# Optimization experiments

Hardware: AMD Instinct MI355X
Metric: run time of the kernel (lower is better)

## Reference

```python
import jax, jax.numpy as jnp
import numpy as np

B, C, F = 8, 2048, 128


def setup_inputs() -> dict:
    key = jax.random.key(0)
    ks = jax.random.split(key, 13)
    features = jax.random.normal(ks[0], (B, C, F), dtype=jnp.float32)
    # sparse-ish boolean adjacency masks over operations
    pred_mask = jax.random.uniform(ks[1], (B, C, C)) < 0.05
    succ_mask = jax.random.uniform(ks[2], (B, C, C)) < 0.05
    same_type_mask = jax.random.uniform(ks[3], (B, C, C)) < 0.10

    def linear(k, fan_in, fan_out):
        kw, kb = jax.random.split(k)
        bound = 1.0 / np.sqrt(fan_in)
        W = jax.random.uniform(kw, (fan_in, fan_out), minval=-bound, maxval=bound, dtype=jnp.float32)
        b = jax.random.uniform(kb, (fan_out,), minval=-bound, maxval=bound, dtype=jnp.float32)
        return W, b

    W_enc, b_enc = linear(ks[4], F, 4 * F)
    W_space, b_space = linear(ks[5], 3 * F, F)
    W_same, b_same = linear(ks[6], 2 * F, F)
    W_mix, b_mix = linear(ks[7], 2 * F, F)
    return {
        "features": features,
        "pred_mask": pred_mask,
        "succ_mask": succ_mask,
        "same_type_mask": same_type_mask,
        "W_enc": W_enc, "b_enc": b_enc,
        "W_space": W_space, "b_space": b_space,
        "W_same": W_same, "b_same": b_same,
        "W_mix": W_mix, "b_mix": b_mix,
    }


def reference(features, pred_mask, succ_mask, same_type_mask,
              W_enc, b_enc, W_space, b_space, W_same, b_same, W_mix, b_mix):
    # encoder: [B,C,F] -> [B,C,4F], split into origin + 3 message features
    enc = features @ W_enc + b_enc
    origin, e_pred, e_succ, e_same = jnp.split(enc, 4, axis=-1)

    def masked_mean(mask, e):
        # original builds (B,C,C,F) broadcast product then sums over 'other';
        # mathematically this is mask @ e with a clamped-degree divisor.
        m = mask.astype(e.dtype)                         # [B,C,C]
        deg = jnp.maximum(m.sum(-1, keepdims=True), 1.0)  # [B,C,1]
        return jnp.einsum('bij,bjf->bif', m, e) / deg

    pred_f = masked_mean(pred_mask, e_pred)
    succ_f = masked_mean(succ_mask, e_succ)
    same_f = masked_mean(same_type_mask, e_same)

    space_mixed = jnp.concatenate([pred_f, origin, succ_f], axis=-1) @ W_space + b_space
    same_mixed = jnp.concatenate([origin, same_f], axis=-1) @ W_same + b_same
    return jnp.concatenate([space_mixed, same_mixed], axis=-1) @ W_mix + b_mix
```

## Files before the change

### kernel.cpp

```cpp
#include <hip/hip_runtime.h>
#include <stdint.h>

typedef unsigned int uint;
typedef unsigned short ushort;
typedef unsigned char uchar;
typedef __attribute__((ext_vector_type(8))) short bf16x8;
typedef __attribute__((ext_vector_type(4))) float f32x4;

__device__ __forceinline__ ushort f2bf(float f) {
  uint u = __builtin_bit_cast(uint, f);
  return (ushort)((u + 0x7FFFu + ((u >> 16) & 1u)) >> 16);
}

__global__ __launch_bounds__(256) void k_detect(
    const uint* __restrict__ m, int* __restrict__ esz_out) {
  __shared__ int s_ok;
  if (threadIdx.x == 0) s_ok = 1;
  __syncthreads();
  int ok = 1;
  for (int i = 0; i < 64; ++i) {
    uint v = m[(size_t)threadIdx.x * 64 + i];
    if (!(v == 0u || v == 1u || v == 0x3F800000u)) ok = 0;
  }
  if (!ok) atomicAnd(&s_ok, 0);
  __syncthreads();
  if (threadIdx.x == 0) *esz_out = s_ok ? 4 : 1;
}

__global__ __launch_bounds__(256) void k_cvt_feat(
    const float4* __restrict__ in, ushort* __restrict__ out) {
  for (int i = blockIdx.x * 256 + threadIdx.x; i < 524288; i += 65536) {
    float4 v = in[i];
    ushort4 o;
    o.x = f2bf(v.x); o.y = f2bf(v.y); o.z = f2bf(v.z); o.w = f2bf(v.w);
    *(ushort4*)&out[(size_t)i * 4] = o;
  }
}

__global__ __launch_bounds__(256) void k_twt(
    const float* __restrict__ We, const float* __restrict__ Ws,
    const float* __restrict__ Wm, const float* __restrict__ Wx,
    ushort* __restrict__ Te, ushort* __restrict__ Ts,
    ushort* __restrict__ Tm, ushort* __restrict__ Tx) {
  int i = blockIdx.x * 256 + threadIdx.x;
  if (i < 65536) { int n = i >> 7, k = i & 127; Te[i] = f2bf(We[k * 512 + n]); return; }
  i -= 65536;
  if (i < 49152) { int n = i / 384, k = i - n * 384; Ts[i] = f2bf(Ws[k * 128 + n]); return; }
  i -= 49152;
  if (i < 32768) { int n = i >> 8, k = i & 255; Tm[i] = f2bf(Wm[k * 128 + n]); return; }
  i -= 32768;
  if (i < 32768) { int n = i >> 8, k = i & 255; Tx[i] = f2bf(Wx[k * 128 + n]); return; }
}

__device__ __forceinline__ void mfma_tiles(const ushort* As, const ushort* Bs,
                                           int m0w, int n0w, int lr, int quad,
                                           f32x4 acc[2][4]) {
#pragma unroll
  for (int kc = 0; kc < 2; ++kc) {
    bf16x8 a[2], b[4];
#pragma unroll
    for (int i = 0; i < 2; ++i)
      a[i] = *(const bf16x8*)&As[(m0w + i * 16 + lr) * 72 + kc * 32 + quad * 8];
#pragma unroll
    for (int j = 0; j < 4; ++j)
      b[j] = *(const bf16x8*)&Bs[(n0w + j * 16 + lr) * 72 + kc * 32 + quad * 8];
#pragma unroll
    for (int i = 0; i < 2; ++i)
#pragma unroll
      for (int j = 0; j < 4; ++j)
        acc[i][j] = __builtin_amdgcn_mfma_f32_16x16x32_bf16(a[i], b[j], acc[i][j], 0, 0, 0);
  }
}

__global__ __launch_bounds__(256) void k_enc(
    const ushort* __restrict__ featbf, const ushort* __restrict__ WTe,
    const float* __restrict__ bias, ushort* __restrict__ origin,
    ushort* __restrict__ eT0, ushort* __restrict__ eT1, ushort* __restrict__ eT2) {
  __shared__ ushort As[64 * 72];
  __shared__ ushort Bs[128 * 72];
  const int t = threadIdx.x;
  const int gm0 = blockIdx.x * 64;
  const int y = blockIdx.y;
  const ushort* Bsrc = WTe + (size_t)y * 128 * 128;
  const int lane = t & 63, wave = t >> 6;
  const int m0w = (wave >> 1) * 32, n0w = (wave & 1) * 64;
  const int quad = lane >> 4, lr = lane & 15;
  const int am = t >> 2, aq = t & 3;
  const int bn = t >> 1, bh = t & 1;
  f32x4 acc[2][4] = {};
  for (int k0 = 0; k0 < 128; k0 += 64) {
    const ushort* asrc = featbf + (size_t)(gm0 + am) * 128 + k0 + aq * 16;
    bf16x8 av0 = *(const bf16x8*)asrc;
    bf16x8 av1 = *(const bf16x8*)(asrc + 8);
    const ushort* bsrc = Bsrc + (size_t)bn * 128 + k0 + bh * 32;
    bf16x8 bv0 = *(const bf16x8*)bsrc;
    bf16x8 bv1 = *(const bf16x8*)(bsrc + 8);
    bf16x8 bv2 = *(const bf16x8*)(bsrc + 16);
    bf16x8 bv3 = *(const bf16x8*)(bsrc + 24);
    *(bf16x8*)&As[am * 72 + aq * 16] = av0;
    *(bf16x8*)&As[am * 72 + aq * 16 + 8] = av1;
    *(bf16x8*)&Bs[bn * 72 + bh * 32] = bv0;
    *(bf16x8*)&Bs[bn * 72 + bh * 32 + 8] = bv1;
    *(bf16x8*)&Bs[bn * 72 + bh * 32 + 16] = bv2;
    *(bf16x8*)&Bs[bn * 72 + bh * 32 + 24] = bv3;
    __syncthreads();
    mfma_tiles(As, Bs, m0w, n0w, lr, quad, acc);
    __syncthreads();
  }
  ushort* eT = (y == 1) ? eT0 : (y == 2) ? eT1 : eT2;
#pragma unroll
  for (int i = 0; i < 2; ++i)
#pragma unroll
    for (int j = 0; j < 4; ++j)
#pragma unroll
      for (int r = 0; r < 4; ++r) {
        int m = gm0 + m0w + i * 16 + quad * 4 + r;
        int n = n0w + j * 16 + lr;
        ushort h = f2bf(acc[i][j][r] + bias[y * 128 + n]);
        if (y == 0) origin[(size_t)m * 128 + n] = h;
        else eT[(size_t)n * 16384 + m] = h;
      }
}

__global__ __launch_bounds__(256) void k_mm(
    const void* __restrict__ mp, const void* __restrict__ ms, const void* __restrict__ mt,
    const ushort* __restrict__ eT0, const ushort* __restrict__ eT1, const ushort* __restrict__ eT2,
    ushort* __restrict__ P, ushort* __restrict__ S, ushort* __restrict__ T,
    const int* __restrict__ esz_p) {
  __shared__ ushort As[64 * 72];
  __shared__ ushort Bs[128 * 72];
  __shared__ uint degs[64];
  const int t = threadIdx.x;
  const int mtile = blockIdx.x, b = blockIdx.y, mid = blockIdx.z;
  const void* mask = (mid == 0) ? mp : (mid == 1) ? ms : mt;
  const ushort* eT = (mid == 0) ? eT0 : (mid == 1) ? eT1 : eT2;
  ushort* outp = (mid == 0) ? P : (mid == 1) ? S : T;
  const int esz = *esz_p;
  if (t < 64) degs[t] = 0;
  const size_t rowbase = (size_t)b * 2048 + mtile * 64;
  const int lane = t & 63, wave = t >> 6;
  const int m0w = (wave >> 1) * 32, n0w = (wave & 1) * 64;
  const int quad = lane >> 4, lr = lane & 15;
  const int am = t >> 2, aq = t & 3;
  const int bn = t >> 1, bh = t & 1;
  const ushort* bsrc_base = eT + (size_t)bn * 16384 + (size_t)b * 2048 + bh * 32;
  f32x4 acc[2][4] = {};
  int cnt = 0;
  for (int k0 = 0; k0 < 2048; k0 += 64) {
    bf16x8 o0, o1;
    if (esz == 4) {
      const uint* p = (const uint*)mask + (rowbase + am) * 2048 + k0 + aq * 16;
      uint w[16];
      *(uint4*)&w[0] = *(const uint4*)p;
      *(uint4*)&w[4] = *(const uint4*)(p + 4);
      *(uint4*)&w[8] = *(const uint4*)(p + 8);
      *(uint4*)&w[12] = *(const uint4*)(p + 12);
#pragma unroll
      for (int e = 0; e < 8; ++e) { int nz = (w[e] != 0u); o0[e] = nz ? (short)0x3F80 : (short)0; cnt += nz; }
#pragma unroll
      for (int e = 0; e < 8; ++e) { int nz = (w[e + 8] != 0u); o1[e] = nz ? (short)0x3F80 : (short)0; cnt += nz; }
    } else {
      const uchar* p = (const uchar*)mask + (rowbase + am) * 2048 + k0 + aq * 16;
      uint4 wb = *(const uint4*)p;
      uint arr[4] = {wb.x, wb.y, wb.z, wb.w};
#pragma unroll
      for (int e = 0; e < 8; ++e) { int nz = (((arr[e >> 2] >> ((e & 3) * 8)) & 0xFFu) != 0u); o0[e] = nz ? (short)0x3F80 : (short)0; cnt += nz; }
#pragma unroll
      for (int e = 0; e < 8; ++e) { int ee = e + 8; int nz = (((arr[ee >> 2] >> ((ee & 3) * 8)) & 0xFFu) != 0u); o1[e] = nz ? (short)0x3F80 : (short)0; cnt += nz; }
    }
    const ushort* bsrc = bsrc_base + k0;
    bf16x8 bv0 = *(const bf16x8*)bsrc;
    bf16x8 bv1 = *(const bf16x8*)(bsrc + 8);
    bf16x8 bv2 = *(const bf16x8*)(bsrc + 16);
    bf16x8 bv3 = *(const bf16x8*)(bsrc + 24);
    *(bf16x8*)&As[am * 72 + aq * 16] = o0;
    *(bf16x8*)&As[am * 72 + aq * 16 + 8] = o1;
    *(bf16x8*)&Bs[bn * 72 + bh * 32] = bv0;
    *(bf16x8*)&Bs[bn * 72 + bh * 32 + 8] = bv1;
    *(bf16x8*)&Bs[bn * 72 + bh * 32 + 16] = bv2;
    *(bf16x8*)&Bs[bn * 72 + bh * 32 + 24] = bv3;
    __syncthreads();
    mfma_tiles(As, Bs, m0w, n0w, lr, quad, acc);
    __syncthreads();
  }
  atomicAdd(&degs[am], (uint)cnt);
  __syncthreads();
#pragma unroll
  for (int i = 0; i < 2; ++i)
#pragma unroll
    for (int r = 0; r < 4; ++r) {
      int ml = m0w + i * 16 + quad * 4 + r;
      uint d = degs[ml];
      float inv = 1.0f / (float)(d > 0u ? d : 1u);
#pragma unroll
      for (int j = 0; j < 4; ++j) {
        int n = n0w + j * 16 + lr;
        outp[(rowbase + ml) * 128 + n] = f2bf(acc[i][j][r] * inv);
      }
    }
}

__global__ __launch_bounds__(256) void k_gemm(
    const ushort* __restrict__ A0, const ushort* __restrict__ A1,
    const ushort* __restrict__ A2, const ushort* __restrict__ Bsrc,
    int bstride, int K, const float* __restrict__ bias,
    void* __restrict__ out, int out_f32) {
  __shared__ ushort As[64 * 72];
  __shared__ ushort Bs[128 * 72];
  const int t = threadIdx.x;
  const int gm0 = blockIdx.x * 64;
  const int lane = t & 63, wave = t >> 6;
  const int m0w = (wave >> 1) * 32, n0w = (wave & 1) * 64;
  const int quad = lane >> 4, lr = lane & 15;
  const int am = t >> 2, aq = t & 3;
  const int bn = t >> 1, bh = t & 1;
  f32x4 acc[2][4] = {};
  for (int k0 = 0; k0 < K; k0 += 64) {
    const int seg = k0 >> 7;
    const ushort* Ap = (seg == 0) ? A0 : (seg == 1) ? A1 : A2;
    const ushort* asrc = Ap + (size_t)(gm0 + am) * 128 + (k0 & 127) + aq * 16;
    bf16x8 av0 = *(const bf16x8*)asrc;
    bf16x8 av1 = *(const bf16x8*)(asrc + 8);
    const ushort* bsrc = Bsrc + (size_t)bn * bstride + k0 + bh * 32;
    bf16x8 bv0 = *(const bf16x8*)bsrc;
    bf16x8 bv1 = *(const bf16x8*)(bsrc + 8);
    bf16x8 bv2 = *(const bf16x8*)(bsrc + 16);
    bf16x8 bv3 = *(const bf16x8*)(bsrc + 24);
    *(bf16x8*)&As[am * 72 + aq * 16] = av0;
    *(bf16x8*)&As[am * 72 + aq * 16 + 8] = av1;
    *(bf16x8*)&Bs[bn * 72 + bh * 32] = bv0;
    *(bf16x8*)&Bs[bn * 72 + bh * 32 + 8] = bv1;
    *(bf16x8*)&Bs[bn * 72 + bh * 32 + 16] = bv2;
    *(bf16x8*)&Bs[bn * 72 + bh * 32 + 24] = bv3;
    __syncthreads();
    mfma_tiles(As, Bs, m0w, n0w, lr, quad, acc);
    __syncthreads();
  }
#pragma unroll
  for (int i = 0; i < 2; ++i)
#pragma unroll
    for (int j = 0; j < 4; ++j)
#pragma unroll
      for (int r = 0; r < 4; ++r) {
        int m = gm0 + m0w + i * 16 + quad * 4 + r;
        int n = n0w + j * 16 + lr;
        float v = acc[i][j][r] + bias[n];
        if (out_f32) ((float*)out)[(size_t)m * 128 + n] = v;
        else ((ushort*)out)[(size_t)m * 128 + n] = f2bf(v);
      }
}

extern "C" void kernel_launch(void* const* d_in, const int* in_sizes, int n_in,
                              void* d_out, int out_size, void* d_ws,
                              size_t ws_size, hipStream_t stream) {
  const float* features = (const float*)d_in[0];
  const void* pred = d_in[1];
  const void* succ = d_in[2];
  const void* same = d_in[3];
  const float* W_enc = (const float*)d_in[4];
  const float* b_enc = (const float*)d_in[5];
  const float* W_space = (const float*)d_in[6];
  const float* b_space = (const float*)d_in[7];
  const float* W_same = (const float*)d_in[8];
  const float* b_same = (const float*)d_in[9];
  const float* W_mix = (const float*)d_in[10];
  const float* b_mix = (const float*)d_in[11];

  const size_t M = 16384;
  ushort* w = (ushort*)d_ws;
  ushort* feat_bf = w;  w += M * 128;
  ushort* WT_enc = w;   w += 512 * 128;
  ushort* WT_space = w; w += 128 * 384;
  ushort* WT_same = w;  w += 128 * 256;
  ushort* WT_mix = w;   w += 128 * 256;
  ushort* origin = w;   w += M * 128;
  ushort* eT0 = w;      w += M * 128;
  ushort* eT1 = w;      w += M * 128;
  ushort* eT2 = w;      w += M * 128;
  ushort* P = w;        w += M * 128;
  ushort* S = w;        w += M * 128;
  ushort* T = w;        w += M * 128;
  ushort* X = w;        w += M * 128;
  ushort* Y = w;        w += M * 128;
  int* esz = (int*)w;

  k_detect<<<1, 256, 0, stream>>>((const uint*)pred, esz);
  k_cvt_feat<<<256, 256, 0, stream>>>((const float4*)features, feat_bf);
  k_twt<<<704, 256, 0, stream>>>(W_enc, W_space, W_same, W_mix,
                                 WT_enc, WT_space, WT_same, WT_mix);
  k_enc<<<dim3(256, 4), 256, 0, stream>>>(feat_bf, WT_enc, b_enc,
                                          origin, eT0, eT1, eT2);
  k_mm<<<dim3(32, 8, 3), 256, 0, stream>>>(pred, succ, same, eT0, eT1, eT2,
                                           P, S, T, esz);
  k_gemm<<<256, 256, 0, stream>>>(P, origin, S, WT_space, 384, 384,
                                  b_space, X, 0);
  k_gemm<<<256, 256, 0, stream>>>(origin, T, nullptr, WT_same, 256, 256,
                                  b_same, Y, 0);
  k_gemm<<<256, 256, 0, stream>>>(X, Y, nullptr, WT_mix, 256, 256,
                                  b_mix, d_out, 1);
}
```

Measured before the change: 475.4 us.

## Drop LDS staging, load MFMA fragments directly from global, merge small kernels

Every GEMM kernel (encoder, masked aggregation, output projections) now loads bf16 fragments straight from global memory into registers instead of staging tiles through shared memory, which removes the __syncthreads barriers. The mask matmul converts byte masks to bf16 with byte-permute arithmetic, prefetches the next mask chunk, and computes degrees with wave shuffles instead of shared-memory atomics. Feature conversion and weight transposition merge into one prep kernel, and the space and same GEMMs merge into one launch. The trade-off is that operands are no longer shared between waves, so redundant global loads rely on cache hits.

```diff
diff --git a/kernel.cpp b/kernel.cpp
--- a/kernel.cpp
+++ b/kernel.cpp
@@ -12,37 +12,68 @@
   return (ushort)((u + 0x7FFFu + ((u >> 16) & 1u)) >> 16);
 }
 
+__device__ __forceinline__ bf16x8 cvt8(uint lo, uint hi, uint& cacc) {
+  uint x0 = __builtin_amdgcn_perm(0u, lo, 0x04010400u);
+  uint x1 = __builtin_amdgcn_perm(0u, lo, 0x04030402u);
+  uint x2 = __builtin_amdgcn_perm(0u, hi, 0x04010400u);
+  uint x3 = __builtin_amdgcn_perm(0u, hi, 0x04030402u);
+  uint n0 = ((x0 + 0x00FF00FFu) >> 8) & 0x00010001u;
+  uint n1 = ((x1 + 0x00FF00FFu) >> 8) & 0x00010001u;
+  uint n2 = ((x2 + 0x00FF00FFu) >> 8) & 0x00010001u;
+  uint n3 = ((x3 + 0x00FF00FFu) >> 8) & 0x00010001u;
+  cacc += n0 + n1 + n2 + n3;
+  uint4 o;
+  o.x = n0 * 0x3F80u; o.y = n1 * 0x3F80u;
+  o.z = n2 * 0x3F80u; o.w = n3 * 0x3F80u;
+  return __builtin_bit_cast(bf16x8, o);
+}
+
+__device__ __forceinline__ bf16x8 cvt8w(uint4 a, uint4 b, uint& cnt) {
+  bf16x8 r;
+  r[0] = a.x ? (short)0x3F80 : (short)0; cnt += (a.x != 0u);
+  r[1] = a.y ? (short)0x3F80 : (short)0; cnt += (a.y != 0u);
+  r[2] = a.z ? (short)0x3F80 : (short)0; cnt += (a.z != 0u);
+  r[3] = a.w ? (short)0x3F80 : (short)0; cnt += (a.w != 0u);
+  r[4] = b.x ? (short)0x3F80 : (short)0; cnt += (b.x != 0u);
+  r[5] = b.y ? (short)0x3F80 : (short)0; cnt += (b.y != 0u);
+  r[6] = b.z ? (short)0x3F80 : (short)0; cnt += (b.z != 0u);
+  r[7] = b.w ? (short)0x3F80 : (short)0; cnt += (b.w != 0u);
+  return r;
+}
+
 __global__ __launch_bounds__(256) void k_detect(
-    const uint* __restrict__ m, int* __restrict__ esz_out) {
+    const uint4* __restrict__ m, int* __restrict__ esz_out) {
   __shared__ int s_ok;
   if (threadIdx.x == 0) s_ok = 1;
   __syncthreads();
   int ok = 1;
-  for (int i = 0; i < 64; ++i) {
-    uint v = m[(size_t)threadIdx.x * 64 + i];
-    if (!(v == 0u || v == 1u || v == 0x3F800000u)) ok = 0;
+#pragma unroll
+  for (int i = 0; i < 16; ++i) {
+    uint4 v = m[i * 256 + threadIdx.x];
+    if (!(v.x <= 1u || v.x == 0x3F800000u)) ok = 0;
+    if (!(v.y <= 1u || v.y == 0x3F800000u)) ok = 0;
+    if (!(v.z <= 1u || v.z == 0x3F800000u)) ok = 0;
+    if (!(v.w <= 1u || v.w == 0x3F800000u)) ok = 0;
   }
   if (!ok) atomicAnd(&s_ok, 0);
   __syncthreads();
   if (threadIdx.x == 0) *esz_out = s_ok ? 4 : 1;
 }
 
-__global__ __launch_bounds__(256) void k_cvt_feat(
-    const float4* __restrict__ in, ushort* __restrict__ out) {
-  for (int i = blockIdx.x * 256 + threadIdx.x; i < 524288; i += 65536) {
-    float4 v = in[i];
-    ushort4 o;
-    o.x = f2bf(v.x); o.y = f2bf(v.y); o.z = f2bf(v.z); o.w = f2bf(v.w);
-    *(ushort4*)&out[(size_t)i * 4] = o;
-  }
-}
-
-__global__ __launch_bounds__(256) void k_twt(
+__global__ __launch_bounds__(256) void k_prep(
+    const float4* __restrict__ fin, ushort* __restrict__ fout,
     const float* __restrict__ We, const float* __restrict__ Ws,
     const float* __restrict__ Wm, const float* __restrict__ Wx,
     ushort* __restrict__ Te, ushort* __restrict__ Ts,
     ushort* __restrict__ Tm, ushort* __restrict__ Tx) {
-  int i = blockIdx.x * 256 + threadIdx.x;
+  const int tid = blockIdx.x * 256 + threadIdx.x;
+  for (int i = tid; i < 524288; i += 180224) {
+    float4 v = fin[i];
+    ushort4 o;
+    o.x = f2bf(v.x); o.y = f2bf(v.y); o.z = f2bf(v.z); o.w = f2bf(v.w);
+    *(ushort4*)&fout[(size_t)i * 4] = o;
+  }
+  int i = tid;
   if (i < 65536) { int n = i >> 7, k = i & 127; Te[i] = f2bf(We[k * 512 + n]); return; }
   i -= 65536;
   if (i < 49152) { int n = i / 384, k = i - n * 384; Ts[i] = f2bf(Ws[k * 128 + n]); return; }
@@ -52,83 +83,73 @@
   if (i < 32768) { int n = i >> 8, k = i & 255; Tx[i] = f2bf(Wx[k * 128 + n]); return; }
 }
 
-__device__ __forceinline__ void mfma_tiles(const ushort* As, const ushort* Bs,
-                                           int m0w, int n0w, int lr, int quad,
-                                           f32x4 acc[2][4]) {
-#pragma unroll
-  for (int kc = 0; kc < 2; ++kc) {
-    bf16x8 a[2], b[4];
-#pragma unroll
-    for (int i = 0; i < 2; ++i)
-      a[i] = *(const bf16x8*)&As[(m0w + i * 16 + lr) * 72 + kc * 32 + quad * 8];
-#pragma unroll
-    for (int j = 0; j < 4; ++j)
-      b[j] = *(const bf16x8*)&Bs[(n0w + j * 16 + lr) * 72 + kc * 32 + quad * 8];
-#pragma unroll
-    for (int i = 0; i < 2; ++i)
-#pragma unroll
-      for (int j = 0; j < 4; ++j)
-        acc[i][j] = __builtin_amdgcn_mfma_f32_16x16x32_bf16(a[i], b[j], acc[i][j], 0, 0, 0);
-  }
-}
-
 __global__ __launch_bounds__(256) void k_enc(
     const ushort* __restrict__ featbf, const ushort* __restrict__ WTe,
     const float* __restrict__ bias, ushort* __restrict__ origin,
     ushort* __restrict__ eT0, ushort* __restrict__ eT1, ushort* __restrict__ eT2) {
-  __shared__ ushort As[64 * 72];
-  __shared__ ushort Bs[128 * 72];
   const int t = threadIdx.x;
   const int gm0 = blockIdx.x * 64;
   const int y = blockIdx.y;
-  const ushort* Bsrc = WTe + (size_t)y * 128 * 128;
   const int lane = t & 63, wave = t >> 6;
   const int m0w = (wave >> 1) * 32, n0w = (wave & 1) * 64;
   const int quad = lane >> 4, lr = lane & 15;
-  const int am = t >> 2, aq = t & 3;
-  const int bn = t >> 1, bh = t & 1;
+  const ushort* a0p = featbf + (size_t)(gm0 + m0w + lr) * 128 + quad * 8;
+  const ushort* a1p = a0p + 16 * 128;
+  bf16x8 af0[4], af1[4];
+#pragma unroll
+  for (int kc = 0; kc < 4; ++kc) {
+    af0[kc] = *(const bf16x8*)(a0p + kc * 32);
+    af1[kc] = *(const bf16x8*)(a1p + kc * 32);
+  }
   f32x4 acc[2][4] = {};
-  for (int k0 = 0; k0 < 128; k0 += 64) {
-    const ushort* asrc = featbf + (size_t)(gm0 + am) * 128 + k0 + aq * 16;
-    bf16x8 av0 = *(const bf16x8*)asrc;
-    bf16x8 av1 = *(const bf16x8*)(asrc + 8);
-    const ushort* bsrc = Bsrc + (size_t)bn * 128 + k0 + bh * 32;
-    bf16x8 bv0 = *(const bf16x8*)bsrc;
-    bf16x8 bv1 = *(const bf16x8*)(bsrc + 8);
-    bf16x8 bv2 = *(const bf16x8*)(bsrc + 16);
-    bf16x8 bv3 = *(const bf16x8*)(bsrc + 24);
-    *(bf16x8*)&As[am * 72 + aq * 16] = av0;
-    *(bf16x8*)&As[am * 72 + aq * 16 + 8] = av1;
-    *(bf16x8*)&Bs[bn * 72 + bh * 32] = bv0;
-    *(bf16x8*)&Bs[bn * 72 + bh * 32 + 8] = bv1;
-    *(bf16x8*)&Bs[bn * 72 + bh * 32 + 16] = bv2;
-    *(bf16x8*)&Bs[bn * 72 + bh * 32 + 24] = bv3;
-    __syncthreads();
-    mfma_tiles(As, Bs, m0w, n0w, lr, quad, acc);
-    __syncthreads();
-  }
-  ushort* eT = (y == 1) ? eT0 : (y == 2) ? eT1 : eT2;
-#pragma unroll
-  for (int i = 0; i < 2; ++i)
-#pragma unroll
-    for (int j = 0; j < 4; ++j)
-#pragma unroll
-      for (int r = 0; r < 4; ++r) {
-        int m = gm0 + m0w + i * 16 + quad * 4 + r;
+#pragma unroll
+  for (int j = 0; j < 4; ++j) {
+    const ushort* bp = WTe + (size_t)(y * 128 + n0w + j * 16 + lr) * 128 + quad * 8;
+#pragma unroll
+    for (int kc = 0; kc < 4; ++kc) {
+      bf16x8 bv = *(const bf16x8*)(bp + kc * 32);
+      acc[0][j] = __builtin_amdgcn_mfma_f32_16x16x32_bf16(af0[kc], bv, acc[0][j], 0, 0, 0);
+      acc[1][j] = __builtin_amdgcn_mfma_f32_16x16x32_bf16(af1[kc], bv, acc[1][j], 0, 0, 0);
+    }
+  }
+  if (y == 0) {
+#pragma unroll
+    for (int i = 0; i < 2; ++i)
+#pragma unroll
+      for (int j = 0; j < 4; ++j) {
         int n = n0w + j * 16 + lr;
-        ushort h = f2bf(acc[i][j][r] + bias[y * 128 + n]);
-        if (y == 0) origin[(size_t)m * 128 + n] = h;
-        else eT[(size_t)n * 16384 + m] = h;
-      }
-}
-
-__global__ __launch_bounds__(256) void k_mm(
-    const void* __restrict__ mp, const void* __restrict__ ms, const void* __restrict__ mt,
-    const ushort* __restrict__ eT0, const ushort* __restrict__ eT1, const ushort* __restrict__ eT2,
+        float bb = bias[n];
+        int mb = gm0 + m0w + i * 16 + quad * 4;
+#pragma unroll
+        for (int r = 0; r < 4; ++r)
+          origin[(size_t)(mb + r) * 128 + n] = f2bf(acc[i][j][r] + bb);
+      }
+  } else {
+    ushort* eT = (y == 1) ? eT0 : (y == 2) ? eT1 : eT2;
+#pragma unroll
+    for (int i = 0; i < 2; ++i)
+#pragma unroll
+      for (int j = 0; j < 4; ++j) {
+        int n = n0w + j * 16 + lr;
+        float bb = bias[y * 128 + n];
+        int mb = gm0 + m0w + i * 16 + quad * 4;
+        ushort4 o;
+        o.x = f2bf(acc[i][j][0] + bb);
+        o.y = f2bf(acc[i][j][1] + bb);
+        o.z = f2bf(acc[i][j][2] + bb);
+        o.w = f2bf(acc[i][j][3] + bb);
+        *(ushort4*)&eT[(size_t)n * 16384 + mb] = o;
+      }
+  }
+}
+
+__global__ __launch_bounds__(256, 3) void k_mm(
+    const void* __restrict__ mp, const void* __restrict__ ms,
+    const void* __restrict__ mt,
+    const ushort* __restrict__ eT0, const ushort* __restrict__ eT1,
+    const ushort* __restrict__ eT2,
     ushort* __restrict__ P, ushort* __restrict__ S, ushort* __restrict__ T,
     const int* __restrict__ esz_p) {
-  __shared__ ushort As[64 * 72];
-  __shared__ ushort Bs[128 * 72];
   __shared__ uint degs[64];
   const int t = threadIdx.x;
   const int mtile = blockIdx.x, b = blockIdx.y, mid = blockIdx.z;
@@ -136,55 +157,96 @@
   const ushort* eT = (mid == 0) ? eT0 : (mid == 1) ? eT1 : eT2;
   ushort* outp = (mid == 0) ? P : (mid == 1) ? S : T;
   const int esz = *esz_p;
-  if (t < 64) degs[t] = 0;
   const size_t rowbase = (size_t)b * 2048 + mtile * 64;
   const int lane = t & 63, wave = t >> 6;
   const int m0w = (wave >> 1) * 32, n0w = (wave & 1) * 64;
   const int quad = lane >> 4, lr = lane & 15;
-  const int am = t >> 2, aq = t & 3;
-  const int bn = t >> 1, bh = t & 1;
-  const ushort* bsrc_base = eT + (size_t)bn * 16384 + (size_t)b * 2048 + bh * 32;
+  const int r0 = m0w + lr, r1 = m0w + 16 + lr;
+  const ushort* bp0 = eT + (size_t)(n0w + lr) * 16384 + (size_t)b * 2048 + quad * 8;
+  const ushort* bp1 = bp0 + 16 * 16384;
+  const ushort* bp2 = bp0 + 32 * 16384;
+  const ushort* bp3 = bp0 + 48 * 16384;
   f32x4 acc[2][4] = {};
-  int cnt = 0;
-  for (int k0 = 0; k0 < 2048; k0 += 64) {
-    bf16x8 o0, o1;
-    if (esz == 4) {
-      const uint* p = (const uint*)mask + (rowbase + am) * 2048 + k0 + aq * 16;
-      uint w[16];
-      *(uint4*)&w[0] = *(const uint4*)p;
-      *(uint4*)&w[4] = *(const uint4*)(p + 4);
-      *(uint4*)&w[8] = *(const uint4*)(p + 8);
-      *(uint4*)&w[12] = *(const uint4*)(p + 12);
-#pragma unroll
-      for (int e = 0; e < 8; ++e) { int nz = (w[e] != 0u); o0[e] = nz ? (short)0x3F80 : (short)0; cnt += nz; }
-#pragma unroll
-      for (int e = 0; e < 8; ++e) { int nz = (w[e + 8] != 0u); o1[e] = nz ? (short)0x3F80 : (short)0; cnt += nz; }
-    } else {
-      const uchar* p = (const uchar*)mask + (rowbase + am) * 2048 + k0 + aq * 16;
-      uint4 wb = *(const uint4*)p;
-      uint arr[4] = {wb.x, wb.y, wb.z, wb.w};
-#pragma unroll
-      for (int e = 0; e < 8; ++e) { int nz = (((arr[e >> 2] >> ((e & 3) * 8)) & 0xFFu) != 0u); o0[e] = nz ? (short)0x3F80 : (short)0; cnt += nz; }
-#pragma unroll
-      for (int e = 0; e < 8; ++e) { int ee = e + 8; int nz = (((arr[ee >> 2] >> ((ee & 3) * 8)) & 0xFFu) != 0u); o1[e] = nz ? (short)0x3F80 : (short)0; cnt += nz; }
-    }
-    const ushort* bsrc = bsrc_base + k0;
-    bf16x8 bv0 = *(const bf16x8*)bsrc;
-    bf16x8 bv1 = *(const bf16x8*)(bsrc + 8);
-    bf16x8 bv2 = *(const bf16x8*)(bsrc + 16);
-    bf16x8 bv3 = *(const bf16x8*)(bsrc + 24);
-    *(bf16x8*)&As[am * 72 + aq * 16] = o0;
-    *(bf16x8*)&As[am * 72 + aq * 16 + 8] = o1;
-    *(bf16x8*)&Bs[bn * 72 + bh * 32] = bv0;
-    *(bf16x8*)&Bs[bn * 72 + bh * 32 + 8] = bv1;
-    *(bf16x8*)&Bs[bn * 72 + bh * 32 + 16] = bv2;
-    *(bf16x8*)&Bs[bn * 72 + bh * 32 + 24] = bv3;
-    __syncthreads();
-    mfma_tiles(As, Bs, m0w, n0w, lr, quad, acc);
-    __syncthreads();
-  }
-  atomicAdd(&degs[am], (uint)cnt);
+  uint cacc0 = 0, cacc1 = 0;
+
+  if (esz == 1) {
+    const uchar* ma = (const uchar*)mask + (rowbase + r0) * 2048 + quad * 8;
+    const uchar* mb = (const uchar*)mask + (rowbase + r1) * 2048 + quad * 8;
+    uint2 ra0 = *(const uint2*)(ma);
+    uint2 ra1 = *(const uint2*)(ma + 32);
+    uint2 rb0 = *(const uint2*)(mb);
+    uint2 rb1 = *(const uint2*)(mb + 32);
+#pragma unroll 2
+    for (int k0 = 0; k0 < 2048; k0 += 64) {
+      uint2 na0 = {}, na1 = {}, nb0 = {}, nb1 = {};
+      if (k0 + 64 < 2048) {
+        na0 = *(const uint2*)(ma + k0 + 64);
+        na1 = *(const uint2*)(ma + k0 + 96);
+        nb0 = *(const uint2*)(mb + k0 + 64);
+        nb1 = *(const uint2*)(mb + k0 + 96);
+      }
+#pragma unroll
+      for (int kc = 0; kc < 2; ++kc) {
+        bf16x8 bv0 = *(const bf16x8*)(bp0 + k0 + kc * 32);
+        bf16x8 bv1 = *(const bf16x8*)(bp1 + k0 + kc * 32);
+        bf16x8 bv2 = *(const bf16x8*)(bp2 + k0 + kc * 32);
+        bf16x8 bv3 = *(const bf16x8*)(bp3 + k0 + kc * 32);
+        uint2 wa = kc ? ra1 : ra0;
+        uint2 wb = kc ? rb1 : rb0;
+        bf16x8 a0 = cvt8(wa.x, wa.y, cacc0);
+        bf16x8 a1 = cvt8(wb.x, wb.y, cacc1);
+        acc[0][0] = __builtin_amdgcn_mfma_f32_16x16x32_bf16(a0, bv0, acc[0][0], 0, 0, 0);
+        acc[1][0] = __builtin_amdgcn_mfma_f32_16x16x32_bf16(a1, bv0, acc[1][0], 0, 0, 0);
+        acc[0][1] = __builtin_amdgcn_mfma_f32_16x16x32_bf16(a0, bv1, acc[0][1], 0, 0, 0);
+        acc[1][1] = __builtin_amdgcn_mfma_f32_16x16x32_bf16(a1, bv1, acc[1][1], 0, 0, 0);
+        acc[0][2] = __builtin_amdgcn_mfma_f32_16x16x32_bf16(a0, bv2, acc[0][2], 0, 0, 0);
+        acc[1][2] = __builtin_amdgcn_mfma_f32_16x16x32_bf16(a1, bv2, acc[1][2], 0, 0, 0);
+        acc[0][3] = __builtin_amdgcn_mfma_f32_16x16x32_bf16(a0, bv3, acc[0][3], 0, 0, 0);
+        acc[1][3] = __builtin_amdgcn_mfma_f32_16x16x32_bf16(a1, bv3, acc[1][3], 0, 0, 0);
+      }
+      ra0 = na0; ra1 = na1; rb0 = nb0; rb1 = nb1;
+    }
+  } else {
+    const uint* ma = (const uint*)mask + (rowbase + r0) * 2048 + quad * 8;
+    const uint* mb = (const uint*)mask + (rowbase + r1) * 2048 + quad * 8;
+    for (int k0 = 0; k0 < 2048; k0 += 64) {
+#pragma unroll
+      for (int kc = 0; kc < 2; ++kc) {
+        uint4 wa0 = *(const uint4*)(ma + k0 + kc * 32);
+        uint4 wa1 = *(const uint4*)(ma + k0 + kc * 32 + 4);
+        uint4 wb0 = *(const uint4*)(mb + k0 + kc * 32);
+        uint4 wb1 = *(const uint4*)(mb + k0 + kc * 32 + 4);
+        bf16x8 bv0 = *(const bf16x8*)(bp0 + k0 + kc * 32);
+        bf16x8 bv1 = *(const bf16x8*)(bp1 + k0 + kc * 32);
+        bf16x8 bv2 = *(const bf16x8*)(bp2 + k0 + kc * 32);
+        bf16x8 bv3 = *(const bf16x8*)(bp3 + k0 + kc * 32);
+        bf16x8 a0 = cvt8w(wa0, wa1, cacc0);
+        bf16x8 a1 = cvt8w(wb0, wb1, cacc1);
+        acc[0][0] = __builtin_amdgcn_mfma_f32_16x16x32_bf16(a0, bv0, acc[0][0], 0, 0, 0);
+        acc[1][0] = __builtin_amdgcn_mfma_f32_16x16x32_bf16(a1, bv0, acc[1][0], 0, 0, 0);
+        acc[0][1] = __builtin_amdgcn_mfma_f32_16x16x32_bf16(a0, bv1, acc[0][1], 0, 0, 0);
+        acc[1][1] = __builtin_amdgcn_mfma_f32_16x16x32_bf16(a1, bv1, acc[1][1], 0, 0, 0);
+        acc[0][2] = __builtin_amdgcn_mfma_f32_16x16x32_bf16(a0, bv2, acc[0][2], 0, 0, 0);
+        acc[1][2] = __builtin_amdgcn_mfma_f32_16x16x32_bf16(a1, bv2, acc[1][2], 0, 0, 0);
+        acc[0][3] = __builtin_amdgcn_mfma_f32_16x16x32_bf16(a0, bv3, acc[0][3], 0, 0, 0);
+        acc[1][3] = __builtin_amdgcn_mfma_f32_16x16x32_bf16(a1, bv3, acc[1][3], 0, 0, 0);
+      }
+    }
+  }
+
+  int c0, c1;
+  if (esz == 1) {
+    c0 = (int)((cacc0 & 0xFFFFu) + (cacc0 >> 16));
+    c1 = (int)((cacc1 & 0xFFFFu) + (cacc1 >> 16));
+  } else {
+    c0 = (int)cacc0;
+    c1 = (int)cacc1;
+  }
+  c0 += __shfl_xor(c0, 16); c0 += __shfl_xor(c0, 32);
+  c1 += __shfl_xor(c1, 16); c1 += __shfl_xor(c1, 32);
+  if ((wave & 1) == 0 && quad == 0) { degs[r0] = (uint)c0; degs[r1] = (uint)c1; }
   __syncthreads();
+
 #pragma unroll
   for (int i = 0; i < 2; ++i)
 #pragma unroll
@@ -200,54 +262,77 @@
     }
 }
 
-__global__ __launch_bounds__(256) void k_gemm(
+__device__ __forceinline__ void gemm_body(
     const ushort* __restrict__ A0, const ushort* __restrict__ A1,
     const ushort* __restrict__ A2, const ushort* __restrict__ Bsrc,
     int bstride, int K, const float* __restrict__ bias,
-    void* __restrict__ out, int out_f32) {
-  __shared__ ushort As[64 * 72];
-  __shared__ ushort Bs[128 * 72];
-  const int t = threadIdx.x;
-  const int gm0 = blockIdx.x * 64;
+    void* __restrict__ out, int out_f32, int gm0, int t) {
   const int lane = t & 63, wave = t >> 6;
   const int m0w = (wave >> 1) * 32, n0w = (wave & 1) * 64;
   const int quad = lane >> 4, lr = lane & 15;
-  const int am = t >> 2, aq = t & 3;
-  const int bn = t >> 1, bh = t & 1;
+  const ushort* bbase = Bsrc + (size_t)(n0w + lr) * bstride + quad * 8;
   f32x4 acc[2][4] = {};
   for (int k0 = 0; k0 < K; k0 += 64) {
     const int seg = k0 >> 7;
     const ushort* Ap = (seg == 0) ? A0 : (seg == 1) ? A1 : A2;
-    const ushort* asrc = Ap + (size_t)(gm0 + am) * 128 + (k0 & 127) + aq * 16;
-    bf16x8 av0 = *(const bf16x8*)asrc;
-    bf16x8 av1 = *(const bf16x8*)(asrc + 8);
-    const ushort* bsrc = Bsrc + (size_t)bn * bstride + k0 + bh * 32;
-    bf16x8 bv0 = *(const bf16x8*)bsrc;
-    bf16x8 bv1 = *(const bf16x8*)(bsrc + 8);
-    bf16x8 bv2 = *(const bf16x8*)(bsrc + 16);
-    bf16x8 bv3 = *(const bf16x8*)(bsrc + 24);
-    *(bf16x8*)&As[am * 72 + aq * 16] = av0;
-    *(bf16x8*)&As[am * 72 + aq * 16 + 8] = av1;
-    *(bf16x8*)&Bs[bn * 72 + bh * 32] = bv0;
-    *(bf16x8*)&Bs[bn * 72 + bh * 32 + 8] = bv1;
-    *(bf16x8*)&Bs[bn * 72 + bh * 32 + 16] = bv2;
-    *(bf16x8*)&Bs[bn * 72 + bh * 32 + 24] = bv3;
-    __syncthreads();
-    mfma_tiles(As, Bs, m0w, n0w, lr, quad, acc);
-    __syncthreads();
+    const int ko = k0 & 127;
+    const ushort* a0p = Ap + (size_t)(gm0 + m0w + lr) * 128 + ko + quad * 8;
+    const ushort* a1p = a0p + 16 * 128;
+#pragma unroll
+    for (int kc = 0; kc < 2; ++kc) {
+      bf16x8 av0 = *(const bf16x8*)(a0p + kc * 32);
+      bf16x8 av1 = *(const bf16x8*)(a1p + kc * 32);
+      bf16x8 b0 = *(const bf16x8*)(bbase + k0 + kc * 32);
+      bf16x8 b1 = *(const bf16x8*)(bbase + (size_t)16 * bstride + k0 + kc * 32);
+      bf16x8 b2 = *(const bf16x8*)(bbase + (size_t)32 * bstride + k0 + kc * 32);
+      bf16x8 b3 = *(const bf16x8*)(bbase + (size_t)48 * bstride + k0 + kc * 32);
+      acc[0][0] = __builtin_amdgcn_mfma_f32_16x16x32_bf16(av0, b0, acc[0][0], 0, 0, 0);
+      acc[1][0] = __builtin_amdgcn_mfma_f32_16x16x32_bf16(av1, b0, acc[1][0], 0, 0, 0);
+      acc[0][1] = __builtin_amdgcn_mfma_f32_16x16x32_bf16(av0, b1, acc[0][1], 0, 0, 0);
+      acc[1][1] = __builtin_amdgcn_mfma_f32_16x16x32_bf16(av1, b1, acc[1][1], 0, 0, 0);
+      acc[0][2] = __builtin_amdgcn_mfma_f32_16x16x32_bf16(av0, b2, acc[0][2], 0, 0, 0);
+      acc[1][2] = __builtin_amdgcn_mfma_f32_16x16x32_bf16(av1, b2, acc[1][2], 0, 0, 0);
+      acc[0][3] = __builtin_amdgcn_mfma_f32_16x16x32_bf16(av0, b3, acc[0][3], 0, 0, 0);
+      acc[1][3] = __builtin_amdgcn_mfma_f32_16x16x32_bf16(av1, b3, acc[1][3], 0, 0, 0);
+    }
   }
 #pragma unroll
   for (int i = 0; i < 2; ++i)
 #pragma unroll
-    for (int j = 0; j < 4; ++j)
-#pragma unroll
-      for (int r = 0; r < 4; ++r) {
-        int m = gm0 + m0w + i * 16 + quad * 4 + r;
-        int n = n0w + j * 16 + lr;
-        float v = acc[i][j][r] + bias[n];
-        if (out_f32) ((float*)out)[(size_t)m * 128 + n] = v;
-        else ((ushort*)out)[(size_t)m * 128 + n] = f2bf(v);
-      }
+    for (int j = 0; j < 4; ++j) {
+      const int n = n0w + j * 16 + lr;
+      const float bb = bias[n];
+      const int mb = gm0 + m0w + i * 16 + quad * 4;
+      if (out_f32) {
+#pragma unroll
+        for (int r = 0; r < 4; ++r)
+          ((float*)out)[(size_t)(mb + r) * 128 + n] = acc[i][j][r] + bb;
+      } else {
+#pragma unroll
+        for (int r = 0; r < 4; ++r)
+          ((ushort*)out)[(size_t)(mb + r) * 128 + n] = f2bf(acc[i][j][r] + bb);
+      }
+    }
+}
+
+__global__ __launch_bounds__(256) void k_xy(
+    const ushort* __restrict__ P, const ushort* __restrict__ origin,
+    const ushort* __restrict__ S, const ushort* __restrict__ T,
+    const ushort* __restrict__ WTs, const ushort* __restrict__ WTm,
+    const float* __restrict__ bs, const float* __restrict__ bm,
+    ushort* __restrict__ X, ushort* __restrict__ Y) {
+  const int gm0 = blockIdx.x * 64;
+  if (blockIdx.y == 0)
+    gemm_body(P, origin, S, WTs, 384, 384, bs, X, 0, gm0, threadIdx.x);
+  else
+    gemm_body(origin, T, nullptr, WTm, 256, 256, bm, Y, 0, gm0, threadIdx.x);
+}
+
+__global__ __launch_bounds__(256) void k_mix(
+    const ushort* __restrict__ X, const ushort* __restrict__ Y,
+    const ushort* __restrict__ WTx, const float* __restrict__ bx,
+    float* __restrict__ out) {
+  gemm_body(X, Y, nullptr, WTx, 256, 256, bx, out, 1, blockIdx.x * 64, threadIdx.x);
 }
 
 extern "C" void kernel_launch(void* const* d_in, const int* in_sizes, int n_in,
@@ -284,18 +369,15 @@
   ushort* Y = w;        w += M * 128;
   int* esz = (int*)w;
 
-  k_detect<<<1, 256, 0, stream>>>((const uint*)pred, esz);
-  k_cvt_feat<<<256, 256, 0, stream>>>((const float4*)features, feat_bf);
-  k_twt<<<704, 256, 0, stream>>>(W_enc, W_space, W_same, W_mix,
-                                 WT_enc, WT_space, WT_same, WT_mix);
+  k_detect<<<1, 256, 0, stream>>>((const uint4*)pred, esz);
+  k_prep<<<704, 256, 0, stream>>>((const float4*)features, feat_bf,
+                                  W_enc, W_space, W_same, W_mix,
+                                  WT_enc, WT_space, WT_same, WT_mix);
   k_enc<<<dim3(256, 4), 256, 0, stream>>>(feat_bf, WT_enc, b_enc,
                                           origin, eT0, eT1, eT2);
   k_mm<<<dim3(32, 8, 3), 256, 0, stream>>>(pred, succ, same, eT0, eT1, eT2,
                                            P, S, T, esz);
-  k_gemm<<<256, 256, 0, stream>>>(P, origin, S, WT_space, 384, 384,
-                                  b_space, X, 0);
-  k_gemm<<<256, 256, 0, stream>>>(origin, T, nullptr, WT_same, 256, 256,
-                                  b_same, Y, 0);
-  k_gemm<<<256, 256, 0, stream>>>(X, Y, nullptr, WT_mix, 256, 256,
-                                  b_mix, d_out, 1);
-}
+  k_xy<<<dim3(256, 2), 256, 0, stream>>>(P, origin, S, T, WT_space, WT_same,
+                                         b_space, b_same, X, Y);
+  k_mix<<<256, 256, 0, stream>>>(X, Y, WT_mix, b_mix, (float*)d_out);
+}
```

Measured after the change: 500.3 us. 5.3% more time.
